# Optimization experiments

Hardware: AMD Instinct MI355X
Metric: run time of the kernel (lower is better)

The kernel has to match this reference:

```python
import jax, jax.numpy as jnp
import numpy as np

SEG = 2048      # segment_length
RATE = 4        # dilated_rate
DIM = 768
LN_EPS = 1e-5


def _sparsify(x):
    # b (l s) d -> b l s d, take every RATE-th within segment, flatten back
    b, L, d = x.shape
    x = x.reshape(b, L // SEG, SEG, d)[:, :, ::RATE]
    return x.reshape(b, -1, d)


def _layernorm(x, gamma, beta):
    mu = jnp.mean(x, axis=-1, keepdims=True)
    var = jnp.mean(jnp.square(x - mu), axis=-1, keepdims=True)
    return (x - mu) / jnp.sqrt(var + LN_EPS) * gamma + beta


def setup_inputs() -> dict:
    key = jax.random.key(0)
    ks = jax.random.split(key, 6)
    B, L, D = 4, 8192, DIM
    return {
        "Q": jax.random.normal(ks[0], (B, L, D), dtype=jnp.float32),
        "K": jax.random.normal(ks[1], (B, L, D), dtype=jnp.float32),
        "V": jax.random.normal(ks[2], (B, L, D), dtype=jnp.float32),
        "Wq": jax.random.normal(ks[3], (D, D), dtype=jnp.float32) * (1.0 / np.sqrt(D)),
        "Wk": jax.random.normal(ks[4], (D, D), dtype=jnp.float32) * (1.0 / np.sqrt(D)),
        "Wv": jax.random.normal(ks[5], (D, D), dtype=jnp.float32) * (1.0 / np.sqrt(D)),
        "ln_gamma": jnp.ones((D,), dtype=jnp.float32),
        "ln_beta": jnp.zeros((D,), dtype=jnp.float32),
    }


def reference(Q, K, V, Wq, Wk, Wv, ln_gamma, ln_beta):
    # strided segment dilation gather
    q = _sparsify(Q)  # [B, Ls, D], Ls = L/SEG * ceil(SEG/RATE)
    k = _sparsify(K)
    v = _sparsify(V)
    # linear projections (torch Linear: y = x @ W.T, no bias)
    q = q @ Wq.T
    k = k @ Wk.T
    v = v @ Wv.T
    # qk LayerNorm (shared norm module)
    q = _layernorm(q, ln_gamma, ln_beta)
    k = _layernorm(k, ln_gamma, ln_beta)
    # scaled dot product attention (non-causal, default scale 1/sqrt(D))
    scale = 1.0 / np.sqrt(q.shape[-1]).astype(np.float32)
    attn = jax.nn.softmax(jnp.einsum('bqd,bkd->bqk', q, k) * scale, axis=-1)
    out = jnp.einsum('bqk,bkd->bqd', attn, v)
    # dropout is identity in eval mode; final softmax over feature dim (as in source)
    return jax.nn.softmax(out, axis=-1)
```

## Files before the change

### kernel.cpp

```cpp
#include <hip/hip_runtime.h>
#include <math.h>

#define SEGLEN 2048
#define SRATE 4
#define DIM 768
#define BATCH 4
#define LFULL 8192
#define LSP 2048
#define NROWS (BATCH * LSP)
#define LN_EPS 1e-5f
#define ATT_SCALE 0.03608439182435161f

typedef __attribute__((ext_vector_type(8))) short s16x8;
typedef __attribute__((ext_vector_type(4))) float f32x4;

__device__ __forceinline__ ushort f2bf(float f) {
    unsigned u = __float_as_uint(f);
    u += 0x7fffu + ((u >> 16) & 1u);
    return (ushort)(u >> 16);
}
__device__ __forceinline__ float bf2f(ushort h) {
    return __uint_as_float(((unsigned)h) << 16);
}

__device__ __forceinline__ void ld_lds16(const ushort* g, ushort* l) {
    __builtin_amdgcn_global_load_lds(
        (const __attribute__((address_space(1))) void*)g,
        (__attribute__((address_space(3))) void*)l, 16, 0, 0);
}

__global__ void pack3(const float* __restrict__ Q, const float* __restrict__ Ks,
                      const float* __restrict__ V, ushort* __restrict__ X) {
    const float* src = blockIdx.z == 0 ? Q : blockIdx.z == 1 ? Ks : V;
    ushort* dst = X + (long)blockIdx.z * (NROWS * DIM);
    int idx = blockIdx.x * 256 + threadIdx.x;
    int r  = idx / (DIM / 4);
    int dg = idx - r * (DIM / 4);
    int bb = r >> 11;
    int s  = r & 2047;
    int seg = s >> 9;
    int j   = s & 511;
    long srow = (long)bb * LFULL + seg * SEGLEN + j * SRATE;
    float4 f = *(const float4*)(src + srow * DIM + dg * 4);
    ushort4 o;
    o.x = f2bf(f.x); o.y = f2bf(f.y); o.z = f2bf(f.z); o.w = f2bf(f.w);
    *(ushort4*)(dst + (long)r * DIM + dg * 4) = o;
}

__global__ void conv3(const float* __restrict__ Wq, const float* __restrict__ Wk,
                      const float* __restrict__ Wv, ushort* __restrict__ W) {
    const float* src = blockIdx.z == 0 ? Wq : blockIdx.z == 1 ? Wk : Wv;
    ushort* dst = W + (long)blockIdx.z * (DIM * DIM);
    int idx = blockIdx.x * 256 + threadIdx.x;
    float4 f = *(const float4*)(src + (long)idx * 4);
    ushort4 o;
    o.x = f2bf(f.x); o.y = f2bf(f.y); o.z = f2bf(f.z); o.w = f2bf(f.w);
    *(ushort4*)(dst + (long)idx * 4) = o;
}

template<int MODE>
__global__ __launch_bounds__(256, 2) void gemm_bt(
    const ushort* __restrict__ Ag, const ushort* __restrict__ Bg,
    ushort* __restrict__ Cb, ushort* __restrict__ Cb2,
    float* __restrict__ Cf, float* __restrict__ Cf2, float* __restrict__ lsum,
    int M, int N, int K, int lda, int ldb, long sA, long sB, long sC,
    int ldc, float scale)
{
    __shared__ ushort lds[2][2][8192];

    const int gx = gridDim.x, gy = gridDim.y;
    const int G = gx * gy * gridDim.z;
    const int f = blockIdx.x + gx * (blockIdx.y + gy * blockIdx.z);
    const int wg = (f & 7) * (G >> 3) + (f >> 3);
    const int bx = wg % gx;
    const int rest = wg / gx;
    const int by = rest % gy;
    const int z  = rest / gy;

    const int bz = (MODE == 3) ? (z >> 1) : z;
    const int hz = (MODE == 3) ? (z & 1) : 0;
    const ushort* Aop = Ag + (long)bz * sA + (long)hz * K;
    const ushort* Bop = Bg + (long)bz * sB + (long)hz * K;

    const int tid = threadIdx.x;
    const int wid = tid >> 6, lane = tid & 63;
    const int wm = wid >> 1, wn = wid & 1;
    const int quad = lane >> 4, lr = lane & 15;
    const int rowBase = by * 128;
    const int colBase = bx * 128;

    int ib = ((lane & 15) << 6) | ((lane >> 4) << 4);
    ib ^= ((ib >> 9) & 1) << 5;

    long offA[4], offB[4];
#pragma unroll
    for (int i = 0; i < 4; i++) {
        int c = i * 256 + tid;
        int cc = c ^ (((c >> 5) & 1) << 1);
        int s = cc >> 6;
        int row  = ((s >> 1) << 4) + ((cc >> 2) & 15);
        int colE = ((s & 1) << 5) + ((cc & 3) << 3);
        offA[i] = (long)(rowBase + row) * lda + colE;
        offB[i] = (long)(colBase + row) * ldb + colE;
    }

    const int NT = K >> 6;

#define STA(buf, vv, i) ld_lds16(Aop + offA[i] + (long)(vv) * 64, &lds[buf][0][(i) * 2048 + wid * 512])
#define STB(buf, vv, i) ld_lds16(Bop + offB[i] + (long)(vv) * 64, &lds[buf][1][(i) * 2048 + wid * 512])

#pragma unroll
    for (int i = 0; i < 4; i++) { STA(0, 0, i); STB(0, 0, i); }
    asm volatile("s_waitcnt vmcnt(0)" ::: "memory");
    __builtin_amdgcn_s_barrier();

    f32x4 acc[4][4] = {};

    for (int v = 0; v < NT; ++v) {
        const int b = v & 1;
        if (v + 1 < NT) {
#pragma unroll
            for (int i = 0; i < 4; i++) { STA(b ^ 1, v + 1, i); STB(b ^ 1, v + 1, i); }
        }
        const char* lA = (const char*)&lds[b][0][0];
        const char* lB = (const char*)&lds[b][1][0];
#pragma unroll
        for (int ks = 0; ks < 2; ++ks) {
            s16x8 af[4], bfm[4];
#pragma unroll
            for (int t = 0; t < 4; ++t)
                af[t] = *(const s16x8*)(lA + (((wm * 4 + t) * 2 + ks) << 10) + ib);
#pragma unroll
            for (int t = 0; t < 4; ++t)
                bfm[t] = *(const s16x8*)(lB + (((wn * 4 + t) * 2 + ks) << 10) + ib);
            __builtin_amdgcn_s_setprio(1);
#pragma unroll
            for (int i = 0; i < 4; i++)
#pragma unroll
                for (int j = 0; j < 4; j++)
                    acc[i][j] = __builtin_amdgcn_mfma_f32_16x16x32_bf16(
                        af[i], bfm[j], acc[i][j], 0, 0, 0);
            __builtin_amdgcn_s_setprio(0);
        }
        if (v + 1 < NT) asm volatile("s_waitcnt vmcnt(0)" ::: "memory");
        __builtin_amdgcn_s_barrier();
    }
#undef STA
#undef STB

    if (MODE == 0) {
        if (z < 2) {
            ushort* Cz = Cb + (long)z * sC;
#pragma unroll
            for (int i = 0; i < 4; i++) {
                int r0 = rowBase + wm * 64 + i * 16 + quad * 4;
#pragma unroll
                for (int j = 0; j < 4; j++) {
                    int c = colBase + wn * 64 + j * 16 + lr;
#pragma unroll
                    for (int reg = 0; reg < 4; reg++)
                        Cz[(long)(r0 + reg) * ldc + c] = f2bf(acc[i][j][reg]);
                }
            }
        } else {
#pragma unroll
            for (int i = 0; i < 4; i++) {
                int r0 = rowBase + wm * 64 + i * 16 + quad * 4;
                int bidx = r0 >> 11;
                int jj = r0 & 2047;
                ushort* Cz = Cb2 + (long)bidx * DIM * LSP;
#pragma unroll
                for (int j = 0; j < 4; j++) {
                    int c = colBase + wn * 64 + j * 16 + lr;
                    ushort4 o;
                    o.x = f2bf(acc[i][j][0]); o.y = f2bf(acc[i][j][1]);
                    o.z = f2bf(acc[i][j][2]); o.w = f2bf(acc[i][j][3]);
                    *(ushort4*)(Cz + (long)c * LSP + jj) = o;
                }
            }
        }
    } else if (MODE == 2) {
        ushort* Cz = Cb + (long)z * sC;
        float* lz = lsum + (long)z * M;
#pragma unroll
        for (int i = 0; i < 4; i++) {
            int r0 = rowBase + wm * 64 + i * 16 + quad * 4;
#pragma unroll
            for (int reg = 0; reg < 4; reg++) {
                float s = 0.f;
#pragma unroll
                for (int j = 0; j < 4; j++) {
                    int c = colBase + wn * 64 + j * 16 + lr;
                    float e = __expf(acc[i][j][reg] * scale);
                    s += e;
                    Cz[(long)(r0 + reg) * ldc + c] = f2bf(e);
                }
                for (int m = 1; m < 16; m <<= 1) s += __shfl_xor(s, m, 64);
                if (lr == 0) atomicAdd(&lz[r0 + reg], s);
            }
        }
    } else {
        float* Cz = (hz ? Cf2 : Cf) + (long)bz * sC;
#pragma unroll
        for (int i = 0; i < 4; i++) {
            int r0 = rowBase + wm * 64 + i * 16 + quad * 4;
#pragma unroll
            for (int j = 0; j < 4; j++) {
                int c = colBase + wn * 64 + j * 16 + lr;
#pragma unroll
                for (int reg = 0; reg < 4; reg++)
                    Cz[(long)(r0 + reg) * ldc + c] = acc[i][j][reg];
            }
        }
    }
}

__global__ __launch_bounds__(256) void ln_inplace(
    ushort* __restrict__ X, const float* __restrict__ gamma,
    const float* __restrict__ beta)
{
    int wid = threadIdx.x >> 6, lane = threadIdx.x & 63;
    int row = blockIdx.x * 4 + wid;
    ushort* xp = X + (long)row * DIM;
    float v[12];
    float s = 0.f;
#pragma unroll
    for (int c = 0; c < 12; c++) { v[c] = bf2f(xp[c * 64 + lane]); s += v[c]; }
    for (int m = 1; m < 64; m <<= 1) s += __shfl_xor(s, m, 64);
    float mean = s * (1.0f / 768.0f);
    float q = 0.f;
#pragma unroll
    for (int c = 0; c < 12; c++) { float d = v[c] - mean; q += d * d; }
    for (int m = 1; m < 64; m <<= 1) q += __shfl_xor(q, m, 64);
    float rstd = rsqrtf(q * (1.0f / 768.0f) + LN_EPS);
#pragma unroll
    for (int c = 0; c < 12; c++) {
        int idx = c * 64 + lane;
        float y = (v[c] - mean) * rstd * gamma[idx] + beta[idx];
        xp[idx] = f2bf(y);
    }
}

__global__ __launch_bounds__(256) void final_softmax(
    const float* __restrict__ O0, const float* __restrict__ O1,
    const float* __restrict__ l, float* __restrict__ out)
{
    int wid = threadIdx.x >> 6, lane = threadIdx.x & 63;
    int row = blockIdx.x * 4 + wid;
    long base = (long)row * DIM;
    float inv = 1.0f / l[row];
    float v[12]; float mx = -1e30f;
#pragma unroll
    for (int c = 0; c < 12; c++) {
        v[c] = (O0[base + c * 64 + lane] + O1[base + c * 64 + lane]) * inv;
        mx = fmaxf(mx, v[c]);
    }
    for (int m = 1; m < 64; m <<= 1) mx = fmaxf(mx, __shfl_xor(mx, m, 64));
    float s = 0.f;
#pragma unroll
    for (int c = 0; c < 12; c++) { v[c] = __expf(v[c] - mx); s += v[c]; }
    for (int m = 1; m < 64; m <<= 1) s += __shfl_xor(s, m, 64);
    float invs = 1.0f / s;
#pragma unroll
    for (int c = 0; c < 12; c++) out[base + c * 64 + lane] = v[c] * invs;
}

extern "C" void kernel_launch(void* const* d_in, const int* in_sizes, int n_in,
                              void* d_out, int out_size, void* d_ws, size_t ws_size,
                              hipStream_t stream)
{
    const float* Q  = (const float*)d_in[0];
    const float* K_ = (const float*)d_in[1];
    const float* V  = (const float*)d_in[2];
    const float* Wq = (const float*)d_in[3];
    const float* Wk = (const float*)d_in[4];
    const float* Wv = (const float*)d_in[5];
    const float* g  = (const float*)d_in[6];
    const float* b  = (const float*)d_in[7];
    float* out = (float*)d_out;

    char* ws = (char*)d_ws;
    ushort* Xq  = (ushort*)(ws + 0);
    ushort* Wqb = (ushort*)(ws + 37748736);
    ushort* qb  = (ushort*)(ws + 41287680);
    ushort* kb  = (ushort*)(ws + 53870592);
    ushort* vT  = (ushort*)(ws + 66453504);
    float*  O0  = (float*)(ws + 79036416);
    float*  l   = (float*)(ws + 104202240);
    ushort* P   = (ushort*)(ws + 0);
    float*  O1  = (float*)(ws + 41287680);

    (void)in_sizes; (void)n_in; (void)out_size; (void)ws_size;

    hipMemsetAsync(l, 0, NROWS * sizeof(float), stream);

    pack3<<<dim3(6144, 1, 3), 256, 0, stream>>>(Q, K_, V, Xq);
    conv3<<<dim3(576, 1, 3), 256, 0, stream>>>(Wq, Wk, Wv, Wqb);

    gemm_bt<0><<<dim3(DIM / 128, NROWS / 128, 3), 256, 0, stream>>>(
        Xq, Wqb, qb, vT, nullptr, nullptr, nullptr,
        NROWS, DIM, DIM, DIM, DIM,
        (long)NROWS * DIM, (long)DIM * DIM, (long)NROWS * DIM, DIM, 0.f);

    ln_inplace<<<4096, 256, 0, stream>>>(qb, g, b);

    gemm_bt<2><<<dim3(LSP / 128, LSP / 128, BATCH), 256, 0, stream>>>(
        qb, kb, P, nullptr, nullptr, nullptr, l,
        LSP, LSP, DIM, DIM, DIM,
        (long)LSP * DIM, (long)LSP * DIM, (long)LSP * LSP, LSP, ATT_SCALE);

    gemm_bt<3><<<dim3(DIM / 128, LSP / 128, BATCH * 2), 256, 0, stream>>>(
        P, vT, nullptr, nullptr, O0, O1, nullptr,
        LSP, DIM, LSP / 2, LSP, LSP,
        (long)LSP * LSP, (long)DIM * LSP, (long)LSP * DIM, DIM, 0.f);

    final_softmax<<<2048, 256, 0, stream>>>(O0, O1, l, out);
}
```

Measured before the change: 377.9 us.

## Fuse QK^T, exp and PV into a single flash-style attention kernel with KV split

Replaces the separate score GEMM (which wrote the bf16 exp matrix P to global memory) and the PV GEMM with one fused kernel. Each block takes a 64-row query tile and a quarter of the keys, computes scores in 128-key chunks, exponentiates them into LDS and multiplies by V^T straight away, accumulating four partial outputs that the final softmax kernel sums. The aim is to drop the global round trip of the large P matrix and one launch. In exchange the Q tile is reloaded for every KV chunk, the partial-output buffer is bigger, and each block holds a large accumulator in registers. Like the old code, it relies on the exp not overflowing because there is no max subtraction.

```diff
diff --git a/kernel.cpp b/kernel.cpp
--- a/kernel.cpp
+++ b/kernel.cpp
@@ -58,13 +58,10 @@
     *(ushort4*)(dst + (long)idx * 4) = o;
 }
 
-template<int MODE>
-__global__ __launch_bounds__(256, 2) void gemm_bt(
+__global__ __launch_bounds__(256, 2) void gemm_proj(
     const ushort* __restrict__ Ag, const ushort* __restrict__ Bg,
     ushort* __restrict__ Cb, ushort* __restrict__ Cb2,
-    float* __restrict__ Cf, float* __restrict__ Cf2, float* __restrict__ lsum,
-    int M, int N, int K, int lda, int ldb, long sA, long sB, long sC,
-    int ldc, float scale)
+    int lda, int ldb, long sA, long sB, long sC, int ldc)
 {
     __shared__ ushort lds[2][2][8192];
 
@@ -77,10 +74,9 @@
     const int by = rest % gy;
     const int z  = rest / gy;
 
-    const int bz = (MODE == 3) ? (z >> 1) : z;
-    const int hz = (MODE == 3) ? (z & 1) : 0;
-    const ushort* Aop = Ag + (long)bz * sA + (long)hz * K;
-    const ushort* Bop = Bg + (long)bz * sB + (long)hz * K;
+    const ushort* Aop = Ag;
+    const ushort* Bop = Bg + (long)z * sB;
+    const ushort* Az  = Aop + (long)z * sA;
 
     const int tid = threadIdx.x;
     const int wid = tid >> 6, lane = tid & 63;
@@ -104,9 +100,9 @@
         offB[i] = (long)(colBase + row) * ldb + colE;
     }
 
-    const int NT = K >> 6;
-
-#define STA(buf, vv, i) ld_lds16(Aop + offA[i] + (long)(vv) * 64, &lds[buf][0][(i) * 2048 + wid * 512])
+    const int NT = DIM >> 6;
+
+#define STA(buf, vv, i) ld_lds16(Az + offA[i] + (long)(vv) * 64, &lds[buf][0][(i) * 2048 + wid * 512])
 #define STB(buf, vv, i) ld_lds16(Bop + offB[i] + (long)(vv) * 64, &lds[buf][1][(i) * 2048 + wid * 512])
 
 #pragma unroll
@@ -148,71 +144,246 @@
 #undef STA
 #undef STB
 
-    if (MODE == 0) {
-        if (z < 2) {
-            ushort* Cz = Cb + (long)z * sC;
-#pragma unroll
-            for (int i = 0; i < 4; i++) {
-                int r0 = rowBase + wm * 64 + i * 16 + quad * 4;
-#pragma unroll
-                for (int j = 0; j < 4; j++) {
-                    int c = colBase + wn * 64 + j * 16 + lr;
-#pragma unroll
-                    for (int reg = 0; reg < 4; reg++)
-                        Cz[(long)(r0 + reg) * ldc + c] = f2bf(acc[i][j][reg]);
-                }
-            }
-        } else {
-#pragma unroll
-            for (int i = 0; i < 4; i++) {
-                int r0 = rowBase + wm * 64 + i * 16 + quad * 4;
-                int bidx = r0 >> 11;
-                int jj = r0 & 2047;
-                ushort* Cz = Cb2 + (long)bidx * DIM * LSP;
-#pragma unroll
-                for (int j = 0; j < 4; j++) {
-                    int c = colBase + wn * 64 + j * 16 + lr;
-                    ushort4 o;
-                    o.x = f2bf(acc[i][j][0]); o.y = f2bf(acc[i][j][1]);
-                    o.z = f2bf(acc[i][j][2]); o.w = f2bf(acc[i][j][3]);
-                    *(ushort4*)(Cz + (long)c * LSP + jj) = o;
-                }
-            }
-        }
-    } else if (MODE == 2) {
+    if (z < 2) {
         ushort* Cz = Cb + (long)z * sC;
-        float* lz = lsum + (long)z * M;
 #pragma unroll
         for (int i = 0; i < 4; i++) {
             int r0 = rowBase + wm * 64 + i * 16 + quad * 4;
 #pragma unroll
-            for (int reg = 0; reg < 4; reg++) {
-                float s = 0.f;
-#pragma unroll
-                for (int j = 0; j < 4; j++) {
-                    int c = colBase + wn * 64 + j * 16 + lr;
-                    float e = __expf(acc[i][j][reg] * scale);
-                    s += e;
-                    Cz[(long)(r0 + reg) * ldc + c] = f2bf(e);
-                }
-                for (int m = 1; m < 16; m <<= 1) s += __shfl_xor(s, m, 64);
-                if (lr == 0) atomicAdd(&lz[r0 + reg], s);
+            for (int j = 0; j < 4; j++) {
+                int c = colBase + wn * 64 + j * 16 + lr;
+#pragma unroll
+                for (int reg = 0; reg < 4; reg++)
+                    Cz[(long)(r0 + reg) * ldc + c] = f2bf(acc[i][j][reg]);
             }
         }
     } else {
-        float* Cz = (hz ? Cf2 : Cf) + (long)bz * sC;
 #pragma unroll
         for (int i = 0; i < 4; i++) {
             int r0 = rowBase + wm * 64 + i * 16 + quad * 4;
+            int bidx = r0 >> 11;
+            int jj = r0 & 2047;
+            ushort* Cz = Cb2 + (long)bidx * DIM * LSP;
 #pragma unroll
             for (int j = 0; j < 4; j++) {
                 int c = colBase + wn * 64 + j * 16 + lr;
+                ushort4 o;
+                o.x = f2bf(acc[i][j][0]); o.y = f2bf(acc[i][j][1]);
+                o.z = f2bf(acc[i][j][2]); o.w = f2bf(acc[i][j][3]);
+                *(ushort4*)(Cz + (long)c * LSP + jj) = o;
+            }
+        }
+    }
+}
+
+__global__ __launch_bounds__(512) void attn_fused(
+    const ushort* __restrict__ qb, const ushort* __restrict__ kb,
+    const ushort* __restrict__ vT, float* __restrict__ Op,
+    float* __restrict__ l)
+{
+    __shared__ ushort P_lds[8192];
+    __shared__ ushort sh[36864];
+
+    const int p = blockIdx.x + 4 * blockIdx.y;
+    const int xcd = p & 7, idx = p >> 3;
+    const int g = xcd + 8 * (idx >> 5);
+    const int m = idx & 31;
+    const int bb = g >> 2, kvq = g & 3;
+    const int qt = bb * 32 + m;
+    const int kv0 = kvq * 512;
+
+    const int tid = threadIdx.x;
+    const int w = tid >> 6, lane = tid & 63;
+    const int wm = w >> 2, wn = w & 3;
+    const int quad = lane >> 4, lr = lane & 15;
+
+    int ib = ((lane & 15) << 6) | ((lane >> 4) << 4);
+    ib ^= ((ib >> 9) & 1) << 5;
+
+    long offQ; long offK[2]; long offV[4];
+    {
+        int c = tid;
+        int cc = c ^ (((c >> 5) & 1) << 1);
+        int s = cc >> 6;
+        int row  = ((s >> 1) << 4) + ((cc >> 2) & 15);
+        int colE = ((s & 1) << 5) + ((cc & 3) << 3);
+        offQ = ((long)(qt * 64 + row)) * DIM + colE;
+#pragma unroll
+        for (int i = 0; i < 2; i++) {
+            int c2 = i * 512 + tid;
+            int cc2 = c2 ^ (((c2 >> 5) & 1) << 1);
+            int s2 = cc2 >> 6;
+            int r2 = ((s2 >> 1) << 4) + ((cc2 >> 2) & 15);
+            int e2 = ((s2 & 1) << 5) + ((cc2 & 3) << 3);
+            offK[i] = (long)r2 * DIM + e2;
+        }
+#pragma unroll
+        for (int i = 0; i < 4; i++) {
+            int c4 = i * 512 + tid;
+            int cc4 = c4 ^ (((c4 >> 5) & 1) << 1);
+            int s4 = cc4 >> 6;
+            int r4 = ((s4 >> 2) << 4) + ((cc4 >> 2) & 15);
+            int e4 = ((s4 & 3) << 5) + ((cc4 & 3) << 3);
+            offV[i] = (long)r4 * LSP + e4;
+        }
+    }
+
+    f32x4 acc_o[6][2][2] = {};
+    float lp[2][4] = {};
+
+    for (int tt = 0; tt < 4; ++tt) {
+        const int kvin = kv0 + tt * 128;
+        const long kbase = ((long)bb * LSP + kvin) * DIM;
+        const long vbase = (long)bb * DIM * LSP + kvin;
+
+        ld_lds16(qb + offQ, sh + w * 512);
+        ld_lds16(kb + kbase + offK[0], sh + 4096 + w * 512);
+        ld_lds16(kb + kbase + offK[1], sh + 8192 + w * 512);
+        ld_lds16(qb + offQ + 64, sh + 12288 + w * 512);
+        ld_lds16(kb + kbase + offK[0] + 64, sh + 12288 + 4096 + w * 512);
+        ld_lds16(kb + kbase + offK[1] + 64, sh + 12288 + 8192 + w * 512);
+        asm volatile("s_waitcnt vmcnt(3)" ::: "memory");
+        __builtin_amdgcn_s_barrier();
+
+        f32x4 acc_s[2][2] = {};
+        int buf = 0;
+        for (int kc = 0; kc < 12; ++kc) {
+            if (kc < 10) {
+                const int nb = (buf == 2) ? 0 : ((buf == 1) ? 2 : 1);
+                const int nb2 = (nb == 2) ? 0 : nb + 1;
+                (void)nb;
+                ld_lds16(qb + offQ + (kc + 2) * 64, sh + nb2 * 12288 + w * 512);
+                ld_lds16(kb + kbase + offK[0] + (kc + 2) * 64, sh + nb2 * 12288 + 4096 + w * 512);
+                ld_lds16(kb + kbase + offK[1] + (kc + 2) * 64, sh + nb2 * 12288 + 8192 + w * 512);
+            } else if (kc == 10) {
+                ld_lds16(vT + vbase + offV[0], sh + w * 512);
+                ld_lds16(vT + vbase + offV[1], sh + 4096 + w * 512);
+            } else {
+                ld_lds16(vT + vbase + offV[2], sh + 8192 + w * 512);
+                ld_lds16(vT + vbase + offV[3], sh + 12288 + w * 512);
+            }
+            const char* lA = (const char*)(sh + buf * 12288);
+            const char* lB = (const char*)(sh + buf * 12288 + 4096);
+            s16x8 aq[2][2], bq[2][2];
+#pragma unroll
+            for (int i = 0; i < 2; i++)
+#pragma unroll
+                for (int ks = 0; ks < 2; ks++)
+                    aq[i][ks] = *(const s16x8*)(lA + (((wm * 2 + i) * 2 + ks) << 10) + ib);
+#pragma unroll
+            for (int j = 0; j < 2; j++)
+#pragma unroll
+                for (int ks = 0; ks < 2; ks++)
+                    bq[j][ks] = *(const s16x8*)(lB + (((wn * 2 + j) * 2 + ks) << 10) + ib);
+            __builtin_amdgcn_s_setprio(1);
+#pragma unroll
+            for (int i = 0; i < 2; i++)
+#pragma unroll
+                for (int j = 0; j < 2; j++)
+#pragma unroll
+                    for (int ks = 0; ks < 2; ks++)
+                        acc_s[i][j] = __builtin_amdgcn_mfma_f32_16x16x32_bf16(
+                            aq[i][ks], bq[j][ks], acc_s[i][j], 0, 0, 0);
+            __builtin_amdgcn_s_setprio(0);
+            if (kc < 10)      asm volatile("s_waitcnt vmcnt(3)" ::: "memory");
+            else if (kc == 10) asm volatile("s_waitcnt vmcnt(2)" ::: "memory");
+            __builtin_amdgcn_s_barrier();
+            buf = (buf == 2) ? 0 : buf + 1;
+        }
+
+        char* Pl = (char*)P_lds;
+#pragma unroll
+        for (int i = 0; i < 2; i++)
+#pragma unroll
+            for (int j = 0; j < 2; j++)
 #pragma unroll
                 for (int reg = 0; reg < 4; reg++)
-                    Cz[(long)(r0 + reg) * ldc + c] = acc[i][j][reg];
-            }
-        }
-    }
+                    acc_s[i][j][reg] = __expf(acc_s[i][j][reg] * ATT_SCALE);
+#pragma unroll
+        for (int i = 0; i < 2; i++)
+#pragma unroll
+            for (int reg = 0; reg < 4; reg++) {
+                float s = acc_s[i][0][reg] + acc_s[i][1][reg];
+                s += __shfl_xor(s, 1, 64);
+                s += __shfl_xor(s, 2, 64);
+                s += __shfl_xor(s, 4, 64);
+                s += __shfl_xor(s, 8, 64);
+                lp[i][reg] += s;
+            }
+#pragma unroll
+        for (int i = 0; i < 2; i++)
+#pragma unroll
+            for (int j = 0; j < 2; j++)
+#pragma unroll
+            for (int reg = 0; reg < 4; reg++) {
+                int r = wm * 32 + i * 16 + quad * 4 + reg;
+                int pb = (r << 8) + ((wn * 32 + j * 16 + lr) << 1);
+                pb ^= (r & 7) << 4;
+                *(ushort*)(Pl + pb) = f2bf(acc_s[i][j][reg]);
+            }
+        __syncthreads();
+
+        s16x8 pa[2][4];
+#pragma unroll
+        for (int i = 0; i < 2; i++)
+#pragma unroll
+            for (int ks = 0; ks < 4; ks++) {
+                int r = wm * 32 + i * 16 + (lane & 15);
+                int pb = (r << 8) + ks * 64 + quad * 16;
+                pb ^= (r & 7) << 4;
+                pa[i][ks] = *(const s16x8*)(Pl + pb);
+            }
+#pragma unroll
+        for (int dc = 0; dc < 6; ++dc) {
+            const int vb = dc & 1;
+            if (dc < 5) {
+                const long vb2 = vbase + (long)((dc + 1) * 128) * LSP;
+#pragma unroll
+                for (int i = 0; i < 4; i++)
+                    ld_lds16(vT + vb2 + offV[i], sh + (vb ^ 1) * 16384 + i * 4096 + w * 512);
+            }
+            const char* lV = (const char*)(sh + vb * 16384);
+            s16x8 vq[2][4];
+#pragma unroll
+            for (int j = 0; j < 2; j++)
+#pragma unroll
+                for (int ks = 0; ks < 4; ks++)
+                    vq[j][ks] = *(const s16x8*)(lV + (((wn * 2 + j) * 4 + ks) << 10) + ib);
+            __builtin_amdgcn_s_setprio(1);
+#pragma unroll
+            for (int i = 0; i < 2; i++)
+#pragma unroll
+                for (int j = 0; j < 2; j++)
+#pragma unroll
+                    for (int ks = 0; ks < 4; ks++)
+                        acc_o[dc][i][j] = __builtin_amdgcn_mfma_f32_16x16x32_bf16(
+                            pa[i][ks], vq[j][ks], acc_o[dc][i][j], 0, 0, 0);
+            __builtin_amdgcn_s_setprio(0);
+            if (dc < 5) asm volatile("s_waitcnt vmcnt(0)" ::: "memory");
+            __builtin_amdgcn_s_barrier();
+        }
+    }
+
+    if (lr == 0) {
+#pragma unroll
+        for (int i = 0; i < 2; i++)
+#pragma unroll
+            for (int reg = 0; reg < 4; reg++)
+                atomicAdd(&l[qt * 64 + wm * 32 + i * 16 + quad * 4 + reg], lp[i][reg]);
+    }
+    float* Out = Op + (long)kvq * NROWS * DIM;
+#pragma unroll
+    for (int dc = 0; dc < 6; ++dc)
+#pragma unroll
+        for (int i = 0; i < 2; i++)
+#pragma unroll
+            for (int j = 0; j < 2; j++)
+#pragma unroll
+                for (int reg = 0; reg < 4; reg++) {
+                    int row = qt * 64 + wm * 32 + i * 16 + quad * 4 + reg;
+                    int col = dc * 128 + wn * 32 + j * 16 + lr;
+                    Out[(long)row * DIM + col] = acc_o[dc][i][j][reg];
+                }
 }
 
 __global__ __launch_bounds__(256) void ln_inplace(
@@ -241,18 +412,20 @@
     }
 }
 
-__global__ __launch_bounds__(256) void final_softmax(
-    const float* __restrict__ O0, const float* __restrict__ O1,
-    const float* __restrict__ l, float* __restrict__ out)
+__global__ __launch_bounds__(256) void final_softmax4(
+    const float* __restrict__ Op, const float* __restrict__ l,
+    float* __restrict__ out)
 {
     int wid = threadIdx.x >> 6, lane = threadIdx.x & 63;
     int row = blockIdx.x * 4 + wid;
     long base = (long)row * DIM;
+    const long ps = (long)NROWS * DIM;
     float inv = 1.0f / l[row];
     float v[12]; float mx = -1e30f;
 #pragma unroll
     for (int c = 0; c < 12; c++) {
-        v[c] = (O0[base + c * 64 + lane] + O1[base + c * 64 + lane]) * inv;
+        long o = base + c * 64 + lane;
+        v[c] = (Op[o] + Op[o + ps] + Op[o + 2 * ps] + Op[o + 3 * ps]) * inv;
         mx = fmaxf(mx, v[c]);
     }
     for (int m = 1; m < 64; m <<= 1) mx = fmaxf(mx, __shfl_xor(mx, m, 64));
@@ -285,10 +458,8 @@
     ushort* qb  = (ushort*)(ws + 41287680);
     ushort* kb  = (ushort*)(ws + 53870592);
     ushort* vT  = (ushort*)(ws + 66453504);
-    float*  O0  = (float*)(ws + 79036416);
-    float*  l   = (float*)(ws + 104202240);
-    ushort* P   = (ushort*)(ws + 0);
-    float*  O1  = (float*)(ws + 41287680);
+    float*  Op  = (float*)(ws + 79036416);
+    float*  l   = (float*)(ws + 179699712);
 
     (void)in_sizes; (void)n_in; (void)out_size; (void)ws_size;
 
@@ -297,22 +468,13 @@
     pack3<<<dim3(6144, 1, 3), 256, 0, stream>>>(Q, K_, V, Xq);
     conv3<<<dim3(576, 1, 3), 256, 0, stream>>>(Wq, Wk, Wv, Wqb);
 
-    gemm_bt<0><<<dim3(DIM / 128, NROWS / 128, 3), 256, 0, stream>>>(
-        Xq, Wqb, qb, vT, nullptr, nullptr, nullptr,
-        NROWS, DIM, DIM, DIM, DIM,
-        (long)NROWS * DIM, (long)DIM * DIM, (long)NROWS * DIM, DIM, 0.f);
+    gemm_proj<<<dim3(DIM / 128, NROWS / 128, 3), 256, 0, stream>>>(
+        Xq, Wqb, qb, vT,
+        DIM, DIM, (long)NROWS * DIM, (long)DIM * DIM, (long)NROWS * DIM, DIM);
 
     ln_inplace<<<4096, 256, 0, stream>>>(qb, g, b);
 
-    gemm_bt<2><<<dim3(LSP / 128, LSP / 128, BATCH), 256, 0, stream>>>(
-        qb, kb, P, nullptr, nullptr, nullptr, l,
-        LSP, LSP, DIM, DIM, DIM,
-        (long)LSP * DIM, (long)LSP * DIM, (long)LSP * LSP, LSP, ATT_SCALE);
-
-    gemm_bt<3><<<dim3(DIM / 128, LSP / 128, BATCH * 2), 256, 0, stream>>>(
-        P, vT, nullptr, nullptr, O0, O1, nullptr,
-        LSP, DIM, LSP / 2, LSP, LSP,
-        (long)LSP * LSP, (long)DIM * LSP, (long)LSP * DIM, DIM, 0.f);
-
-    final_softmax<<<2048, 256, 0, stream>>>(O0, O1, l, out);
-}
+    attn_fused<<<dim3(4, 128), 512, 0, stream>>>(qb, kb, vT, Op, l);
+
+    final_softmax4<<<2048, 256, 0, stream>>>(Op, l, out);
+}
```

Result: slower. 412.2 us (+9.1%).

## Split GEMM K-tile loads into half-stages with finer-grained vmcnt pipelining

Applied to the files above, without the earlier changes.

The shared bf16 GEMM now lays out each 64-wide K tile in LDS as two 32-wide k-halves. It issues the global-to-LDS loads for each half separately and waits with partial vmcnt counts, so the next tile's loads overlap the MFMA work of the current half instead of draining all loads at the end of each tile. The K-tile count becomes a template parameter so the loop bounds are compile-time constants. This adds an extra barrier per tile and makes correctness depend on the exact vmcnt counts and LDS buffer reuse ordering.

```diff
diff --git a/kernel.cpp b/kernel.cpp
--- a/kernel.cpp
+++ b/kernel.cpp
@@ -58,15 +58,16 @@
     *(ushort4*)(dst + (long)idx * 4) = o;
 }
 
-template<int MODE>
+template<int MODE, int NT>
 __global__ __launch_bounds__(256, 2) void gemm_bt(
     const ushort* __restrict__ Ag, const ushort* __restrict__ Bg,
     ushort* __restrict__ Cb, ushort* __restrict__ Cb2,
     float* __restrict__ Cf, float* __restrict__ Cf2, float* __restrict__ lsum,
-    int M, int N, int K, int lda, int ldb, long sA, long sB, long sC,
+    int M, int N, int lda, int ldb, long sA, long sB, long sC,
     int ldc, float scale)
 {
     __shared__ ushort lds[2][2][8192];
+    const int K = NT * 64;
 
     const int gx = gridDim.x, gy = gridDim.y;
     const int G = gx * gy * gridDim.z;
@@ -98,41 +99,42 @@
         int c = i * 256 + tid;
         int cc = c ^ (((c >> 5) & 1) << 1);
         int s = cc >> 6;
-        int row  = ((s >> 1) << 4) + ((cc >> 2) & 15);
-        int colE = ((s & 1) << 5) + ((cc & 3) << 3);
+        int ks = s >> 3, gg = s & 7;
+        int row  = gg * 16 + ((cc >> 2) & 15);
+        int colE = ks * 32 + ((cc & 3) << 3);
         offA[i] = (long)(rowBase + row) * lda + colE;
         offB[i] = (long)(colBase + row) * ldb + colE;
     }
 
-    const int NT = K >> 6;
-
 #define STA(buf, vv, i) ld_lds16(Aop + offA[i] + (long)(vv) * 64, &lds[buf][0][(i) * 2048 + wid * 512])
 #define STB(buf, vv, i) ld_lds16(Bop + offB[i] + (long)(vv) * 64, &lds[buf][1][(i) * 2048 + wid * 512])
 
-#pragma unroll
-    for (int i = 0; i < 4; i++) { STA(0, 0, i); STB(0, 0, i); }
-    asm volatile("s_waitcnt vmcnt(0)" ::: "memory");
-    __builtin_amdgcn_s_barrier();
+    STA(0, 0, 0); STA(0, 0, 1); STB(0, 0, 0); STB(0, 0, 1);
+    STA(0, 0, 2); STA(0, 0, 3); STB(0, 0, 2); STB(0, 0, 3);
+    STA(1, 1, 0); STA(1, 1, 1); STB(1, 1, 0); STB(1, 1, 1);
 
     f32x4 acc[4][4] = {};
 
     for (int v = 0; v < NT; ++v) {
         const int b = v & 1;
-        if (v + 1 < NT) {
-#pragma unroll
-            for (int i = 0; i < 4; i++) { STA(b ^ 1, v + 1, i); STB(b ^ 1, v + 1, i); }
-        }
         const char* lA = (const char*)&lds[b][0][0];
         const char* lB = (const char*)&lds[b][1][0];
-#pragma unroll
-        for (int ks = 0; ks < 2; ++ks) {
+
+        if (v < NT - 1) asm volatile("s_waitcnt vmcnt(8)" ::: "memory");
+        else            asm volatile("s_waitcnt vmcnt(4)" ::: "memory");
+        __builtin_amdgcn_s_barrier();
+        if (v + 1 < NT) {
+            STA(b ^ 1, v + 1, 2); STA(b ^ 1, v + 1, 3);
+            STB(b ^ 1, v + 1, 2); STB(b ^ 1, v + 1, 3);
+        }
+        {
             s16x8 af[4], bfm[4];
 #pragma unroll
             for (int t = 0; t < 4; ++t)
-                af[t] = *(const s16x8*)(lA + (((wm * 4 + t) * 2 + ks) << 10) + ib);
+                af[t] = *(const s16x8*)(lA + ((0 * 8 + wm * 4 + t) << 10) + ib);
 #pragma unroll
             for (int t = 0; t < 4; ++t)
-                bfm[t] = *(const s16x8*)(lB + (((wn * 4 + t) * 2 + ks) << 10) + ib);
+                bfm[t] = *(const s16x8*)(lB + ((0 * 8 + wn * 4 + t) << 10) + ib);
             __builtin_amdgcn_s_setprio(1);
 #pragma unroll
             for (int i = 0; i < 4; i++)
@@ -142,8 +144,31 @@
                         af[i], bfm[j], acc[i][j], 0, 0, 0);
             __builtin_amdgcn_s_setprio(0);
         }
-        if (v + 1 < NT) asm volatile("s_waitcnt vmcnt(0)" ::: "memory");
+
+        if (v < NT - 1) asm volatile("s_waitcnt vmcnt(8)" ::: "memory");
+        else            asm volatile("s_waitcnt vmcnt(0)" ::: "memory");
         __builtin_amdgcn_s_barrier();
+        if (v + 2 < NT) {
+            STA(b, v + 2, 0); STA(b, v + 2, 1);
+            STB(b, v + 2, 0); STB(b, v + 2, 1);
+        }
+        {
+            s16x8 af[4], bfm[4];
+#pragma unroll
+            for (int t = 0; t < 4; ++t)
+                af[t] = *(const s16x8*)(lA + ((1 * 8 + wm * 4 + t) << 10) + ib);
+#pragma unroll
+            for (int t = 0; t < 4; ++t)
+                bfm[t] = *(const s16x8*)(lB + ((1 * 8 + wn * 4 + t) << 10) + ib);
+            __builtin_amdgcn_s_setprio(1);
+#pragma unroll
+            for (int i = 0; i < 4; i++)
+#pragma unroll
+                for (int j = 0; j < 4; j++)
+                    acc[i][j] = __builtin_amdgcn_mfma_f32_16x16x32_bf16(
+                        af[i], bfm[j], acc[i][j], 0, 0, 0);
+            __builtin_amdgcn_s_setprio(0);
+        }
     }
 #undef STA
 #undef STB
@@ -297,21 +322,21 @@
     pack3<<<dim3(6144, 1, 3), 256, 0, stream>>>(Q, K_, V, Xq);
     conv3<<<dim3(576, 1, 3), 256, 0, stream>>>(Wq, Wk, Wv, Wqb);
 
-    gemm_bt<0><<<dim3(DIM / 128, NROWS / 128, 3), 256, 0, stream>>>(
+    gemm_bt<0, 12><<<dim3(DIM / 128, NROWS / 128, 3), 256, 0, stream>>>(
         Xq, Wqb, qb, vT, nullptr, nullptr, nullptr,
-        NROWS, DIM, DIM, DIM, DIM,
+        NROWS, DIM, DIM, DIM,
         (long)NROWS * DIM, (long)DIM * DIM, (long)NROWS * DIM, DIM, 0.f);
 
     ln_inplace<<<4096, 256, 0, stream>>>(qb, g, b);
 
-    gemm_bt<2><<<dim3(LSP / 128, LSP / 128, BATCH), 256, 0, stream>>>(
+    gemm_bt<2, 12><<<dim3(LSP / 128, LSP / 128, BATCH), 256, 0, stream>>>(
         qb, kb, P, nullptr, nullptr, nullptr, l,
-        LSP, LSP, DIM, DIM, DIM,
+        LSP, LSP, DIM, DIM,
         (long)LSP * DIM, (long)LSP * DIM, (long)LSP * LSP, LSP, ATT_SCALE);
 
-    gemm_bt<3><<<dim3(DIM / 128, LSP / 128, BATCH * 2), 256, 0, stream>>>(
+    gemm_bt<3, 16><<<dim3(DIM / 128, LSP / 128, BATCH * 2), 256, 0, stream>>>(
         P, vT, nullptr, nullptr, O0, O1, nullptr,
-        LSP, DIM, LSP / 2, LSP, LSP,
+        LSP, DIM, LSP, LSP,
         (long)LSP * LSP, (long)DIM * LSP, (long)LSP * DIM, DIM, 0.f);
 
     final_softmax<<<2048, 256, 0, stream>>>(O0, O1, l, out);
```

Measured after the change: 383.8 us. No clear change (+1.5%).
